# Optimization experiments

Hardware: AMD Instinct MI355X
Metric: run time of the kernel (lower is better)

Reference implementation:

```python
import jax, jax.numpy as jnp
import numpy as np

N, K, D = 200000, 512, 128


def setup_inputs() -> dict:
    key = jax.random.key(0)
    k1, k2 = jax.random.split(key)
    embs = jax.random.normal(k1, (N, D), dtype=jnp.float32)
    centers = jax.random.normal(k2, (K, D), dtype=jnp.float32)
    return {"embs": embs, "centers": centers}


def _euclidean_cdist(x, c):
    # ||x - c||: stable expansion, avoids [N, K, D] intermediate.
    x2 = jnp.sum(x * x, axis=-1, keepdims=True)        # [N, 1]
    c2 = jnp.sum(c * c, axis=-1)[None, :]              # [1, K]
    xc = jnp.einsum("nd,kd->nk", x, c)                 # [N, K]
    d2 = jnp.maximum(x2 + c2 - 2.0 * xc, 1e-12)
    return jnp.sqrt(d2)


def reference(embs, centers):
    dists = _euclidean_cdist(embs, centers)            # [N, K]
    cluster_dists = jnp.min(dists, axis=1)             # [N] distance to nearest center
    rep_ids = jnp.argmin(dists, axis=0)                # [K] nearest embedding to each center
    loss = jnp.sum(cluster_dists)
    return centers, rep_ids, loss
```

## Files before the change

kernel.cpp:

```cpp
#include <hip/hip_runtime.h>
#include <hip/hip_bf16.h>

typedef __attribute__((ext_vector_type(8)))  short          bf16x8;
typedef __attribute__((ext_vector_type(16))) float          f32x16;
typedef __attribute__((ext_vector_type(8)))  unsigned short u16x8;

#define N_EMB 200000
#define K_C   512
#define D_DIM 128
#define TPB   10
#define NGRPS 625
#define AROW  144
#define BUFB  18432
#define LOOFF 9216
#define MINOFF (2*BUFB)


__device__ __forceinline__ unsigned short bf16_bits(float x) {
    __hip_bfloat16 h = __float2bfloat16(x);
    return *reinterpret_cast<unsigned short*>(&h);
}
__device__ __forceinline__ float bf16_val(unsigned short b) {
    unsigned u = (unsigned)b << 16;
    return __uint_as_float(u);
}

__device__ __forceinline__ int BLK(int g, int n) { return (g << 5) | (n ^ (g & 7)); }

__global__ void init_kernel(const float* __restrict__ centers,
                            unsigned short* __restrict__ hiA,
                            unsigned short* __restrict__ loA,
                            unsigned long long* __restrict__ pack) {
    const int t = threadIdx.x, w = t >> 6, l = t & 63;
    const int k = blockIdx.x * 8 + w;
    const float2 c = *reinterpret_cast<const float2*>(centers + k * D_DIM + 2 * l);
    float c2 = c.x * c.x + c.y * c.y;
#pragma unroll
    for (int off = 1; off < 64; off <<= 1) c2 += __shfl_xor(c2, off);

    float v0 = -2.f * c.x, v1 = -2.f * c.y;
    unsigned short h0 = bf16_bits(v0); unsigned short l0 = bf16_bits(v0 - bf16_val(h0));
    unsigned short h1 = bf16_bits(v1); unsigned short l1 = bf16_bits(v1 - bf16_val(h1));
    *reinterpret_cast<ushort2*>(hiA + k * AROW + 2 * l) = make_ushort2(h0, h1);
    *reinterpret_cast<ushort2*>(loA + k * AROW + 2 * l) = make_ushort2(l0, l1);

    if (l == 0) {
        unsigned short c2h = bf16_bits(c2);
        float c2hf = bf16_val(c2h);
        unsigned short c2l = bf16_bits(c2 - c2hf);
        float c2lf = bf16_val(c2l);
        unsigned short e2c = bf16_bits(c2 - c2hf - c2lf);
        u16x8 a, z;
#pragma unroll
        for (int i = 0; i < 8; ++i) { a[i] = 0; z[i] = 0; }
        a[0] = c2h; a[1] = 0x3F80; a[2] = e2c;
        *reinterpret_cast<u16x8*>(hiA + k * AROW + 128) = a;
        *reinterpret_cast<u16x8*>(hiA + k * AROW + 136) = z;
    }
    if (l == 1) {
        unsigned short c2h = bf16_bits(c2);
        unsigned short c2l = bf16_bits(c2 - bf16_val(c2h));
        u16x8 a, z;
#pragma unroll
        for (int i = 0; i < 8; ++i) { a[i] = 0; z[i] = 0; }
        a[0] = c2l; a[3] = 0x3F80;
        *reinterpret_cast<u16x8*>(loA + k * AROW + 128) = a;
        *reinterpret_cast<u16x8*>(loA + k * AROW + 136) = z;
    }
    if (l == 2) pack[k] = 0xFFFFFFFFFFFFFFFFULL;
}

__launch_bounds__(512, 2)
__global__ void cluster_mfma(const float* __restrict__ embs,
                             const unsigned short* __restrict__ hiA,
                             const unsigned short* __restrict__ loA,
                             unsigned long long* __restrict__ pack,
                             unsigned* __restrict__ minA,
                             unsigned* __restrict__ minB) {
    __shared__ __align__(16) char lds_c[2 * BUFB + TPB * 32 * 4];
    unsigned* minarr = reinterpret_cast<unsigned*>(lds_c + MINOFF);

    const int t = threadIdx.x, w = t >> 6, l = t & 63;
    const int col = l & 31, half = l >> 5;
    const int kside = blockIdx.x & 1, ngrp = blockIdx.x >> 1;
    const int kbase = kside * 256 + w * 32;
    const int myk = kbase + col;
    const int srow = t >> 4, schunk = t & 15;
    const int tbase = ngrp * TPB;

    bf16x8 a_hi[9], a_lo[9];
    {
        const unsigned short* hrow = hiA + myk * AROW + 8 * half;
        const unsigned short* lrow = loA + myk * AROW + 8 * half;
#pragma unroll
        for (int s = 0; s < 9; ++s) {
            a_hi[s] = *reinterpret_cast<const bf16x8*>(hrow + 16 * s);
            a_lo[s] = *reinterpret_cast<const bf16x8*>(lrow + 16 * s);
        }
    }

    float    best_d[16];
    unsigned best_n[16];
#pragma unroll
    for (int r = 0; r < 16; ++r) { best_d[r] = 3.4e38f; best_n[r] = 0u; }

    if (t < TPB * 32) minarr[t] = 0xFFFFFFFFu;

    float vcur[8];
    {
        const float* erow = embs + (tbase * 32 + srow) * D_DIM + schunk * 8;
        float4 u0 = *reinterpret_cast<const float4*>(erow);
        float4 u1 = *reinterpret_cast<const float4*>(erow + 4);
        vcur[0] = u0.x; vcur[1] = u0.y; vcur[2] = u0.z; vcur[3] = u0.w;
        vcur[4] = u1.x; vcur[5] = u1.y; vcur[6] = u1.z; vcur[7] = u1.w;
    }

    for (int tl = 0; tl < TPB; ++tl) {
        char* buf = lds_c + (tl & 1) * BUFB;

        float vnx[8];
        {
            const int tn = (tl < TPB - 1) ? tl + 1 : tl;
            const float* erow = embs + ((tbase + tn) * 32 + srow) * D_DIM + schunk * 8;
            float4 u0 = *reinterpret_cast<const float4*>(erow);
            float4 u1 = *reinterpret_cast<const float4*>(erow + 4);
            vnx[0] = u0.x; vnx[1] = u0.y; vnx[2] = u0.z; vnx[3] = u0.w;
            vnx[4] = u1.x; vnx[5] = u1.y; vnx[6] = u1.z; vnx[7] = u1.w;
        }

        {
            float x2p = 0.f;
            u16x8 hv, lv;
#pragma unroll
            for (int i = 0; i < 8; ++i) {
                float v = vcur[i];
                x2p = fmaf(v, v, x2p);
                unsigned short hb = bf16_bits(v);
                unsigned short lb = bf16_bits(v - bf16_val(hb));
                hv[i] = hb; lv[i] = lb;
            }
            const int wb = BLK(schunk, srow);
            *reinterpret_cast<u16x8*>(buf + (wb << 4)) = hv;
            *reinterpret_cast<u16x8*>(buf + LOOFF + (wb << 4)) = lv;
            float x2 = x2p;
#pragma unroll
            for (int off = 1; off < 16; off <<= 1) x2 += __shfl_xor(x2, off);
            if (schunk == 0) {
                unsigned short x2h = bf16_bits(x2);
                float x2hf = bf16_val(x2h);
                unsigned short x2l = bf16_bits(x2 - x2hf);
                float x2lf = bf16_val(x2l);
                unsigned short e2x = bf16_bits(x2 - x2hf - x2lf);
                u16x8 he, le, z;
#pragma unroll
                for (int i = 0; i < 8; ++i) { he[i] = 0; le[i] = 0; z[i] = 0; }
                he[0] = 0x3F80; he[1] = x2h; he[2] = 0x3F80; he[3] = e2x;
                le[1] = x2l;
                const int b16 = BLK(16, srow), b17 = BLK(17, srow);
                *reinterpret_cast<u16x8*>(buf + (b16 << 4)) = he;
                *reinterpret_cast<u16x8*>(buf + (b17 << 4)) = z;
                *reinterpret_cast<u16x8*>(buf + LOOFF + (b16 << 4)) = le;
                *reinterpret_cast<u16x8*>(buf + LOOFF + (b17 << 4)) = z;
            }
        }
        asm volatile("s_waitcnt lgkmcnt(0)" ::: "memory");
        __builtin_amdgcn_s_barrier();

        f32x16 acc;
#pragma unroll
        for (int r = 0; r < 16; ++r) acc[r] = 0.f;
#pragma unroll
        for (int s = 0; s < 9; ++s) {
            const int gg = (s < 8) ? (2 * s + half) : (16 + half);
            const char* pb = buf + (BLK(gg, col) << 4);
            bf16x8 bh = *reinterpret_cast<const bf16x8*>(pb);
            bf16x8 bl = *reinterpret_cast<const bf16x8*>(pb + LOOFF);
            acc = __builtin_amdgcn_mfma_f32_32x32x16_bf16(a_hi[s], bh, acc, 0, 0, 0);
            acc = __builtin_amdgcn_mfma_f32_32x32x16_bf16(a_hi[s], bl, acc, 0, 0, 0);
            acc = __builtin_amdgcn_mfma_f32_32x32x16_bf16(a_lo[s], bh, acc, 0, 0, 0);
        }

        float m = acc[0];
#pragma unroll
        for (int r = 1; r < 16; ++r) m = fminf(m, acc[r]);
        m = fminf(m, __shfl_xor(m, 32));
        if (l < 32) atomicMin(&minarr[tl * 32 + col], __float_as_uint(m));

        const unsigned ng = (unsigned)((tbase + tl) * 32 + col);
#pragma unroll
        for (int r = 0; r < 16; ++r) {
            bool better = acc[r] < best_d[r];
            best_d[r] = better ? acc[r] : best_d[r];
            best_n[r] = better ? ng : best_n[r];
        }

#pragma unroll
        for (int i = 0; i < 8; ++i) vcur[i] = vnx[i];
    }
    __syncthreads();

    if (t < TPB * 32) {
        unsigned* dst = kside ? minB : minA;
        dst[ngrp * (TPB * 32) + t] = minarr[t];
    }

#pragma unroll
    for (int r = 0; r < 16; ++r) {
        float d = best_d[r];
        unsigned n = best_n[r];
        for (int off = 16; off >= 1; off >>= 1) {
            float od = __shfl_xor(d, off);
            unsigned on = __shfl_xor(n, off);
            bool take = (od < d) || (od == d && on < n);
            d = take ? od : d;
            n = take ? on : n;
        }
        if (col == 0) {
            int k = kbase + (r & 3) + 8 * (r >> 2) + 4 * half;
            unsigned long long p =
                ((unsigned long long)__float_as_uint(d) << 32) | (unsigned long long)n;
            atomicMin(&pack[k], p);
        }
    }
}

__global__ void finalize1(const float* __restrict__ centers,
                          const unsigned long long* __restrict__ pack,
                          const unsigned* __restrict__ minA,
                          const unsigned* __restrict__ minB,
                          float* __restrict__ lossPartial,
                          float* __restrict__ out) {
    __shared__ float wsum[8];
    const int t = threadIdx.x, wv = t >> 6, ln = t & 63;
    const int gid = blockIdx.x * 512 + t;
    if (gid < 16384)
        reinterpret_cast<float4*>(out)[gid] =
            reinterpret_cast<const float4*>(centers)[gid];
    if (gid < K_C)
        out[65536 + gid] = (float)(unsigned)(pack[gid] & 0xFFFFFFFFu);
    float s = 0.f;
    if (gid < N_EMB) {
        float m = fminf(__uint_as_float(minA[gid]), __uint_as_float(minB[gid]));
        s = sqrtf(fmaxf(m, 1e-12f));
    }
#pragma unroll
    for (int off = 1; off < 64; off <<= 1) s += __shfl_xor(s, off);
    if (ln == 0) wsum[wv] = s;
    __syncthreads();
    if (t == 0) {
        float tot = 0.f;
#pragma unroll
        for (int i = 0; i < 8; ++i) tot += wsum[i];
        lossPartial[blockIdx.x] = tot;
    }
}

__global__ void finalize2(const float* __restrict__ lossPartial,
                          float* __restrict__ out) {
    __shared__ float wsum[8];
    const int t = threadIdx.x, wv = t >> 6, ln = t & 63;
    float s = (t < 391) ? lossPartial[t] : 0.f;
#pragma unroll
    for (int off = 1; off < 64; off <<= 1) s += __shfl_xor(s, off);
    if (ln == 0) wsum[wv] = s;
    __syncthreads();
    if (t == 0) {
        float tot = 0.f;
#pragma unroll
        for (int i = 0; i < 8; ++i) tot += wsum[i];
        out[65536 + K_C] = tot;
    }
}

extern "C" void kernel_launch(void* const* d_in, const int* in_sizes, int n_in,
                              void* d_out, int out_size, void* d_ws, size_t ws_size,
                              hipStream_t stream) {
    const float* embs    = (const float*)d_in[0];
    const float* centers = (const float*)d_in[1];
    float* out = (float*)d_out;

    unsigned long long* pack = (unsigned long long*)d_ws;
    unsigned short* hiA = (unsigned short*)((char*)d_ws + 4096);
    unsigned short* loA = (unsigned short*)((char*)d_ws + 151552);
    unsigned* minA = (unsigned*)((char*)d_ws + 299008);
    unsigned* minB = (unsigned*)((char*)d_ws + 1099008);
    float* lossPartial = (float*)((char*)d_ws + 1899008);

    init_kernel<<<64, 512, 0, stream>>>(centers, hiA, loA, pack);
    cluster_mfma<<<NGRPS * 2, 512, 0, stream>>>(embs, hiA, loA, pack, minA, minB);
    finalize1<<<391, 512, 0, stream>>>(centers, pack, minA, minB, lossPartial, out);
    finalize2<<<1, 512, 0, stream>>>(lossPartial, out);
}
```

Baseline: 257.4 us.

## Add norm terms in fp32 epilogue instead of extra MFMA step; pack indices as nibbles

Drops the ninth K-step of the 3-pass bf16 MFMA that folded ||x||² and ||c||² into the dot product. The squared norms now live in LDS tables and are added in fp32 after the MFMA: c² for the per-row minimum, x² for the per-center argmin. Per-center best indices are stored as 4-bit tile numbers in two registers, which frees registers, and launch bounds rise to 4 blocks per CU. The cost is extra per-element adds and LDS reads in the epilogue. A +1024 bias on the packed distance keeps the float-bit ordering valid if values go negative, but it loses some precision.

After: 323.0 us. 25.5% more time.

```diff
diff --git a/kernel.cpp b/kernel.cpp
--- a/kernel.cpp
+++ b/kernel.cpp
@@ -10,10 +10,12 @@
 #define D_DIM 128
 #define TPB   10
 #define NGRPS 625
-#define AROW  144
-#define BUFB  18432
-#define LOOFF 9216
-#define MINOFF (2*BUFB)
+#define BUFB  16384
+#define LOOFF 8192
+#define MINOFF 32768
+#define C2OFF  34048
+#define X2OFF  35072
+#define LDS_TOTAL 35328
 
 
 __device__ __forceinline__ unsigned short bf16_bits(float x) {
@@ -30,6 +32,7 @@
 __global__ void init_kernel(const float* __restrict__ centers,
                             unsigned short* __restrict__ hiA,
                             unsigned short* __restrict__ loA,
+                            float* __restrict__ c2ws,
                             unsigned long long* __restrict__ pack) {
     const int t = threadIdx.x, w = t >> 6, l = t & 63;
     const int k = blockIdx.x * 8 + w;
@@ -41,44 +44,25 @@
     float v0 = -2.f * c.x, v1 = -2.f * c.y;
     unsigned short h0 = bf16_bits(v0); unsigned short l0 = bf16_bits(v0 - bf16_val(h0));
     unsigned short h1 = bf16_bits(v1); unsigned short l1 = bf16_bits(v1 - bf16_val(h1));
-    *reinterpret_cast<ushort2*>(hiA + k * AROW + 2 * l) = make_ushort2(h0, h1);
-    *reinterpret_cast<ushort2*>(loA + k * AROW + 2 * l) = make_ushort2(l0, l1);
-
-    if (l == 0) {
-        unsigned short c2h = bf16_bits(c2);
-        float c2hf = bf16_val(c2h);
-        unsigned short c2l = bf16_bits(c2 - c2hf);
-        float c2lf = bf16_val(c2l);
-        unsigned short e2c = bf16_bits(c2 - c2hf - c2lf);
-        u16x8 a, z;
-#pragma unroll
-        for (int i = 0; i < 8; ++i) { a[i] = 0; z[i] = 0; }
-        a[0] = c2h; a[1] = 0x3F80; a[2] = e2c;
-        *reinterpret_cast<u16x8*>(hiA + k * AROW + 128) = a;
-        *reinterpret_cast<u16x8*>(hiA + k * AROW + 136) = z;
-    }
-    if (l == 1) {
-        unsigned short c2h = bf16_bits(c2);
-        unsigned short c2l = bf16_bits(c2 - bf16_val(c2h));
-        u16x8 a, z;
-#pragma unroll
-        for (int i = 0; i < 8; ++i) { a[i] = 0; z[i] = 0; }
-        a[0] = c2l; a[3] = 0x3F80;
-        *reinterpret_cast<u16x8*>(loA + k * AROW + 128) = a;
-        *reinterpret_cast<u16x8*>(loA + k * AROW + 136) = z;
-    }
-    if (l == 2) pack[k] = 0xFFFFFFFFFFFFFFFFULL;
-}
-
-__launch_bounds__(512, 2)
+    *reinterpret_cast<ushort2*>(hiA + k * D_DIM + 2 * l) = make_ushort2(h0, h1);
+    *reinterpret_cast<ushort2*>(loA + k * D_DIM + 2 * l) = make_ushort2(l0, l1);
+
+    if (l == 0) c2ws[k] = c2;
+    if (l == 1) pack[k] = 0xFFFFFFFFFFFFFFFFULL;
+}
+
+__launch_bounds__(512, 4)
 __global__ void cluster_mfma(const float* __restrict__ embs,
                              const unsigned short* __restrict__ hiA,
                              const unsigned short* __restrict__ loA,
+                             const float* __restrict__ c2ws,
                              unsigned long long* __restrict__ pack,
                              unsigned* __restrict__ minA,
                              unsigned* __restrict__ minB) {
-    __shared__ __align__(16) char lds_c[2 * BUFB + TPB * 32 * 4];
+    __shared__ __align__(16) char lds_c[LDS_TOTAL];
     unsigned* minarr = reinterpret_cast<unsigned*>(lds_c + MINOFF);
+    float*    c2tab  = reinterpret_cast<float*>(lds_c + C2OFF);
+    float*    x2tab  = reinterpret_cast<float*>(lds_c + X2OFF);
 
     const int t = threadIdx.x, w = t >> 6, l = t & 63;
     const int col = l & 31, half = l >> 5;
@@ -88,23 +72,24 @@
     const int srow = t >> 4, schunk = t & 15;
     const int tbase = ngrp * TPB;
 
-    bf16x8 a_hi[9], a_lo[9];
+    bf16x8 a_hi[8], a_lo[8];
     {
-        const unsigned short* hrow = hiA + myk * AROW + 8 * half;
-        const unsigned short* lrow = loA + myk * AROW + 8 * half;
-#pragma unroll
-        for (int s = 0; s < 9; ++s) {
+        const unsigned short* hrow = hiA + myk * D_DIM + 8 * half;
+        const unsigned short* lrow = loA + myk * D_DIM + 8 * half;
+#pragma unroll
+        for (int s = 0; s < 8; ++s) {
             a_hi[s] = *reinterpret_cast<const bf16x8*>(hrow + 16 * s);
             a_lo[s] = *reinterpret_cast<const bf16x8*>(lrow + 16 * s);
         }
     }
 
-    float    best_d[16];
-    unsigned best_n[16];
-#pragma unroll
-    for (int r = 0; r < 16; ++r) { best_d[r] = 3.4e38f; best_n[r] = 0u; }
-
+    if (t < 256) c2tab[t] = c2ws[kside * 256 + t];
     if (t < TPB * 32) minarr[t] = 0xFFFFFFFFu;
+
+    float best_d[16];
+#pragma unroll
+    for (int r = 0; r < 16; ++r) best_d[r] = 3.4e38f;
+    unsigned nib0 = 0u, nib1 = 0u;
 
     float vcur[8];
     {
@@ -117,6 +102,7 @@
 
     for (int tl = 0; tl < TPB; ++tl) {
         char* buf = lds_c + (tl & 1) * BUFB;
+        const int slot = (tl & 1) * 32;
 
         float vnx[8];
         {
@@ -145,23 +131,7 @@
             float x2 = x2p;
 #pragma unroll
             for (int off = 1; off < 16; off <<= 1) x2 += __shfl_xor(x2, off);
-            if (schunk == 0) {
-                unsigned short x2h = bf16_bits(x2);
-                float x2hf = bf16_val(x2h);
-                unsigned short x2l = bf16_bits(x2 - x2hf);
-                float x2lf = bf16_val(x2l);
-                unsigned short e2x = bf16_bits(x2 - x2hf - x2lf);
-                u16x8 he, le, z;
-#pragma unroll
-                for (int i = 0; i < 8; ++i) { he[i] = 0; le[i] = 0; z[i] = 0; }
-                he[0] = 0x3F80; he[1] = x2h; he[2] = 0x3F80; he[3] = e2x;
-                le[1] = x2l;
-                const int b16 = BLK(16, srow), b17 = BLK(17, srow);
-                *reinterpret_cast<u16x8*>(buf + (b16 << 4)) = he;
-                *reinterpret_cast<u16x8*>(buf + (b17 << 4)) = z;
-                *reinterpret_cast<u16x8*>(buf + LOOFF + (b16 << 4)) = le;
-                *reinterpret_cast<u16x8*>(buf + LOOFF + (b17 << 4)) = z;
-            }
+            if (schunk == 0) x2tab[slot + srow] = x2;
         }
         asm volatile("s_waitcnt lgkmcnt(0)" ::: "memory");
         __builtin_amdgcn_s_barrier();
@@ -170,8 +140,8 @@
 #pragma unroll
         for (int r = 0; r < 16; ++r) acc[r] = 0.f;
 #pragma unroll
-        for (int s = 0; s < 9; ++s) {
-            const int gg = (s < 8) ? (2 * s + half) : (16 + half);
+        for (int s = 0; s < 8; ++s) {
+            const int gg = 2 * s + half;
             const char* pb = buf + (BLK(gg, col) << 4);
             bf16x8 bh = *reinterpret_cast<const bf16x8*>(pb);
             bf16x8 bl = *reinterpret_cast<const bf16x8*>(pb + LOOFF);
@@ -180,19 +150,23 @@
             acc = __builtin_amdgcn_mfma_f32_32x32x16_bf16(a_lo[s], bh, acc, 0, 0, 0);
         }
 
-        float m = acc[0];
-#pragma unroll
-        for (int r = 1; r < 16; ++r) m = fminf(m, acc[r]);
+        const float x2c = x2tab[slot + col];
+        const float* c2b = c2tab + w * 32 + 4 * half;
+        float m = 3.4e38f;
+        const unsigned tlu = (unsigned)tl;
+#pragma unroll
+        for (int r = 0; r < 16; ++r) {
+            const float c2k = c2b[(r & 3) + 8 * (r >> 2)];
+            m = fminf(m, acc[r] + c2k);
+            const float drep = acc[r] + x2c;
+            const bool better = drep < best_d[r];
+            best_d[r] = better ? drep : best_d[r];
+            const int sh = 4 * (r & 7);
+            if (r < 8) nib0 = better ? ((nib0 & ~(0xFu << sh)) | (tlu << sh)) : nib0;
+            else       nib1 = better ? ((nib1 & ~(0xFu << sh)) | (tlu << sh)) : nib1;
+        }
         m = fminf(m, __shfl_xor(m, 32));
-        if (l < 32) atomicMin(&minarr[tl * 32 + col], __float_as_uint(m));
-
-        const unsigned ng = (unsigned)((tbase + tl) * 32 + col);
-#pragma unroll
-        for (int r = 0; r < 16; ++r) {
-            bool better = acc[r] < best_d[r];
-            best_d[r] = better ? acc[r] : best_d[r];
-            best_n[r] = better ? ng : best_n[r];
-        }
+        if (l < 32) atomicMin(&minarr[tl * 32 + col], __float_as_uint(m + x2c));
 
 #pragma unroll
         for (int i = 0; i < 8; ++i) vcur[i] = vnx[i];
@@ -207,7 +181,8 @@
 #pragma unroll
     for (int r = 0; r < 16; ++r) {
         float d = best_d[r];
-        unsigned n = best_n[r];
+        const unsigned nib = ((r < 8 ? nib0 : nib1) >> (4 * (r & 7))) & 0xFu;
+        unsigned n = (unsigned)((tbase + (int)nib) * 32 + col);
         for (int off = 16; off >= 1; off >>= 1) {
             float od = __shfl_xor(d, off);
             unsigned on = __shfl_xor(n, off);
@@ -218,7 +193,8 @@
         if (col == 0) {
             int k = kbase + (r & 3) + 8 * (r >> 2) + 4 * half;
             unsigned long long p =
-                ((unsigned long long)__float_as_uint(d) << 32) | (unsigned long long)n;
+                ((unsigned long long)__float_as_uint(d + 1024.f) << 32) |
+                (unsigned long long)n;
             atomicMin(&pack[k], p);
         }
     }
@@ -280,14 +256,15 @@
     float* out = (float*)d_out;
 
     unsigned long long* pack = (unsigned long long*)d_ws;
-    unsigned short* hiA = (unsigned short*)((char*)d_ws + 4096);
-    unsigned short* loA = (unsigned short*)((char*)d_ws + 151552);
-    unsigned* minA = (unsigned*)((char*)d_ws + 299008);
-    unsigned* minB = (unsigned*)((char*)d_ws + 1099008);
-    float* lossPartial = (float*)((char*)d_ws + 1899008);
-
-    init_kernel<<<64, 512, 0, stream>>>(centers, hiA, loA, pack);
-    cluster_mfma<<<NGRPS * 2, 512, 0, stream>>>(embs, hiA, loA, pack, minA, minB);
+    float* c2ws = (float*)((char*)d_ws + 4096);
+    unsigned short* hiA = (unsigned short*)((char*)d_ws + 6144);
+    unsigned short* loA = (unsigned short*)((char*)d_ws + 137216);
+    unsigned* minA = (unsigned*)((char*)d_ws + 268288);
+    unsigned* minB = (unsigned*)((char*)d_ws + 1068288);
+    float* lossPartial = (float*)((char*)d_ws + 1868288);
+
+    init_kernel<<<64, 512, 0, stream>>>(centers, hiA, loA, c2ws, pack);
+    cluster_mfma<<<NGRPS * 2, 512, 0, stream>>>(embs, hiA, loA, c2ws, pack, minA, minB);
     finalize1<<<391, 512, 0, stream>>>(centers, pack, minA, minB, lossPartial, out);
     finalize2<<<1, 512, 0, stream>>>(lossPartial, out);
 }
```
